# Kernel optimization log

Hardware: AMD Instinct MI355X
Metric: run time of the kernel (lower is better)

Reference implementation:

```python
import jax, jax.numpy as jnp
import numpy as np

N = 100000      # rows of edge_features / scatter dim_size
E = 1000000     # edges
C_IN = 16
C_OUT = 16
H = 32
DIM = 3
RADIUS = 1.0
EPS = 1e-5


def setup_inputs() -> dict:
    key = jax.random.key(0)
    ks = jax.random.split(key, 8)
    s1 = 1.0 / np.sqrt(DIM)
    s2 = 1.0 / np.sqrt(H)
    return {
        "in_edges": jax.random.randint(ks[0], (E,), 0, N, dtype=jnp.int32),
        "out_edges": jax.random.randint(ks[1], (E,), 0, N, dtype=jnp.int32),
        "edge_features": jax.random.normal(ks[2], (N, C_IN), dtype=jnp.float32),
        "hood_coords": jax.random.normal(ks[3], (E, DIM), dtype=jnp.float32),
        "W1": jax.random.normal(ks[4], (DIM, H), dtype=jnp.float32) * s1,
        "b1": jnp.zeros((H,), jnp.float32),
        "g1": jnp.ones((H,), jnp.float32),
        "beta1": jnp.zeros((H,), jnp.float32),
        "W2": jax.random.normal(ks[5], (H, H), dtype=jnp.float32) * s2,
        "b2": jnp.zeros((H,), jnp.float32),
        "g2": jnp.ones((H,), jnp.float32),
        "beta2": jnp.zeros((H,), jnp.float32),
        "W3": jax.random.normal(ks[6], (H, C_IN * C_OUT), dtype=jnp.float32) * s2,
        "b3": jnp.zeros((C_IN * C_OUT,), jnp.float32),
    }


def _layernorm(x, g, b):
    m = jnp.mean(x, axis=-1, keepdims=True)
    v = jnp.mean((x - m) ** 2, axis=-1, keepdims=True)
    return (x - m) * jax.lax.rsqrt(v + EPS) * g + b


def reference(in_edges, out_edges, edge_features, hood_coords,
              W1, b1, g1, beta1, W2, b2, g2, beta2, W3, b3):
    # neural field: coords -> per-edge weight matrix [E, C_OUT, C_IN]
    x = hood_coords / RADIUS
    x = jax.nn.relu(_layernorm(x @ W1 + b1, g1, beta1))
    x = jax.nn.relu(_layernorm(x @ W2 + b2, g2, beta2))
    w = jnp.tanh(x @ W3 + b3).reshape(-1, C_OUT, C_IN)
    # gather + per-edge matvec
    f = edge_features[in_edges]                      # [E, C_IN]
    out_ch = jnp.einsum('ni,noi->no', f, w)          # [E, C_OUT]
    # scatter_mean over out_edges with dim_size = N
    sums = jax.ops.segment_sum(out_ch, out_edges, num_segments=N)
    counts = jax.ops.segment_sum(jnp.ones((out_ch.shape[0],), out_ch.dtype),
                                 out_edges, num_segments=N)
    return sums / jnp.maximum(counts, 1.0)[:, None]
```

## Files before the change

kernel.cpp:

```cpp
#include <hip/hip_runtime.h>
#include <hip/hip_bf16.h>


typedef __attribute__((ext_vector_type(4))) short short4v;
typedef __attribute__((ext_vector_type(4))) float float4v;
typedef __attribute__((ext_vector_type(4))) unsigned uint4v;
typedef __attribute__((ext_vector_type(2))) unsigned uint2v;

constexpr float LN_EPS   = 1e-5f;
constexpr float LOG2E_X2 = 2.8853900817779268f;

__device__ __forceinline__ unsigned f2bf(float x) {
  unsigned u = __builtin_bit_cast(unsigned, x);
  u += 0x7FFFu + ((u >> 16) & 1u);
  return u >> 16;
}
__device__ __forceinline__ unsigned pack2(float lo, float hi) {
  return f2bf(lo) | (f2bf(hi) << 16);
}
__device__ __forceinline__ unsigned packc(float lo, float hi) {
  float2 v; v.x = lo; v.y = hi;
  const __hip_bfloat162 b = __float22bfloat162_rn(v);
  static_assert(sizeof(__hip_bfloat162) == 4, "bf16x2 must be 4 bytes");
  unsigned r;
  __builtin_memcpy(&r, &b, 4);
  return r;
}
__device__ __forceinline__ float bflo2f(unsigned u) {
  return __builtin_bit_cast(float, u << 16);
}
__device__ __forceinline__ float bfhi2f(unsigned u) {
  return __builtin_bit_cast(float, u & 0xFFFF0000u);
}

__device__ __forceinline__ float4v mfma16(short4v a, short4v b, float4v c) {
#if __has_builtin(__builtin_amdgcn_mfma_f32_16x16x16bf16_1k)
  return __builtin_amdgcn_mfma_f32_16x16x16bf16_1k(a, b, c, 0, 0, 0);
#else
  float4v d;
  asm volatile("v_mfma_f32_16x16x16_bf16 %0, %1, %2, %3\n\ts_nop 7\n\ts_nop 7"
               : "=&v"(d) : "v"(a), "v"(b), "v"(c));
  return d;
#endif
}

__device__ __forceinline__ void ln_relu_pack(const float* hv, uint4v gp,
                                             uint4v bp, short4v* bh) {
  float sum = 0.f, ss = 0.f;
#pragma unroll
  for (int s = 0; s < 8; ++s) { sum += hv[s]; ss += hv[s] * hv[s]; }
  sum += __shfl_xor(sum, 16);  ss += __shfl_xor(ss, 16);
  sum += __shfl_xor(sum, 32);  ss += __shfl_xor(ss, 32);
  const float m   = sum * (1.0f / 32.0f);
  const float var = fmaxf(ss * (1.0f / 32.0f) - m * m, 0.f);
  const float rs  = rsqrtf(var + LN_EPS);
#pragma unroll
  for (int h = 0; h < 2; ++h) {
    float y[4];
#pragma unroll
    for (int j = 0; j < 4; ++j) {
      const int s = h * 4 + j;
      const float g  = (s & 1) ? bfhi2f(gp[s >> 1]) : bflo2f(gp[s >> 1]);
      const float be = (s & 1) ? bfhi2f(bp[s >> 1]) : bflo2f(bp[s >> 1]);
      y[j] = fmaxf((hv[s] - m) * rs * g + be, 0.f);
    }
    uint2v u;
    u[0] = packc(y[0], y[1]);
    u[1] = packc(y[2], y[3]);
    bh[h] = __builtin_bit_cast(short4v, u);
  }
}


__global__ void nf_hist(const int* __restrict__ out_edges, int* __restrict__ counts, int E) {
  const int t4 = (blockIdx.x * blockDim.x + threadIdx.x) * 4;
  if (t4 + 3 < E) {
    const int4 v = *(const int4*)(out_edges + t4);
    atomicAdd(&counts[v.x], 1);
    atomicAdd(&counts[v.y], 1);
    atomicAdd(&counts[v.z], 1);
    atomicAdd(&counts[v.w], 1);
  } else {
    for (int i = t4; i < E; ++i) atomicAdd(&counts[out_edges[i]], 1);
  }
}

__global__ void nf_alloc(const int* __restrict__ counts, int* __restrict__ offsets,
                         int* __restrict__ cursor, int* __restrict__ total, int N) {
  const int i = blockIdx.x * blockDim.x + threadIdx.x;
  const int lane = threadIdx.x & 63;
  int c = (i < N) ? counts[i] : 0;
  int sc = c;
#pragma unroll
  for (int d = 1; d < 64; d <<= 1) {
    int v = __shfl_up(sc, d);
    if (lane >= d) sc += v;
  }
  const int excl = sc - c;
  const int wtot = __shfl(sc, 63);
  int base = 0;
  if (lane == 0) base = atomicAdd(total, wtot);
  base = __shfl(base, 0);
  if (i < N) {
    offsets[i] = base + excl;
    cursor[i]  = base + excl;
  }
}


template <int SCATTER_MODE>
__global__ __launch_bounds__(256, 2)
void nf_main(const int* __restrict__ in_edges,
             const int* __restrict__ out_edges,
             const float* __restrict__ ef,
             const float* __restrict__ coords,
             const float* __restrict__ W1, const float* __restrict__ b1,
             const float* __restrict__ g1, const float* __restrict__ be1,
             const float* __restrict__ W2, const float* __restrict__ b2,
             const float* __restrict__ g2, const float* __restrict__ be2,
             const float* __restrict__ W3, const float* __restrict__ b3,
             void* __restrict__ out_ch,
             int* __restrict__ aux,
             int* __restrict__ cursor,
             int E, int ntiles)
{
  __shared__ __align__(16) unsigned sA3[16 * 64 * 4];
  __shared__ __align__(16) float    sB3f[16 * 4 * 4];
  __shared__ __align__(16) unsigned sC1[4][16];
  __shared__ __align__(16) unsigned sC2[4][16];
  __shared__ __align__(16) unsigned sC3[4][4];

  const int t    = threadIdx.x;
  const int l    = t & 63;
  const int q    = l >> 4;
  const int ecol = l & 15;

#pragma unroll
  for (int rep = 0; rep < 4; ++rep) {
    const int idx = rep * 256 + t;
    const int o = idx >> 6, ll = idx & 63;
    const int qq = ll >> 4, ec = ll & 15;
    uint4v w;
#pragma unroll
    for (int h = 0; h < 2; ++h)
#pragma unroll
      for (int jp = 0; jp < 2; ++jp) {
        const float lo = LOG2E_X2 * W3[(4 * qq + 2 * jp     + 16 * h) * 256 + o * 16 + ec];
        const float hi = LOG2E_X2 * W3[(4 * qq + 2 * jp + 1 + 16 * h) * 256 + o * 16 + ec];
        w[h * 2 + jp] = pack2(lo, hi);
      }
    *(uint4v*)&sA3[idx * 4] = w;
  }
  if (t < 64) {
    const int o = t >> 2, qq = t & 3;
    float4v bb;
#pragma unroll
    for (int r = 0; r < 4; ++r) bb[r] = LOG2E_X2 * b3[o * 16 + 4 * qq + r];
    *(float4v*)&sB3f[t * 4] = bb;
  }
  if (t < 4) {
    const int qq = t;
#pragma unroll
    for (int i = 0; i < 4; ++i) {
      const int base = (i < 2) ? (4 * qq + 2 * i) : (4 * qq + 16 + 2 * (i - 2));
      sC1[qq][i]      = pack2(W1[base],      W1[base + 1]);
      sC1[qq][4 + i]  = pack2(W1[32 + base], W1[33 + base]);
      sC1[qq][8 + i]  = pack2(W1[64 + base], W1[65 + base]);
      sC1[qq][12 + i] = pack2(b1[base],      b1[base + 1]);
      sC2[qq][i]      = pack2(g1[base],      g1[base + 1]);
      sC2[qq][4 + i]  = pack2(be1[base],     be1[base + 1]);
      sC2[qq][8 + i]  = pack2(g2[base],      g2[base + 1]);
      sC2[qq][12 + i] = pack2(be2[base],     be2[base + 1]);
      sC3[qq][i]      = pack2(b2[base],      b2[base + 1]);
    }
  }

  short4v a2[2][2];
#pragma unroll
  for (int t2 = 0; t2 < 2; ++t2)
#pragma unroll
    for (int h = 0; h < 2; ++h) {
      short4v v;
#pragma unroll
      for (int j = 0; j < 4; ++j)
        v[j] = (short)f2bf(W2[(4 * q + j + 16 * h) * 32 + ecol + 16 * t2]);
      a2[t2][h] = v;
    }

  __syncthreads();

  auto front = [&](float x0, float x1, float x2, short4v* bh) {
    const uint4v w1r0 = *(const uint4v*)&sC1[q][0];
    const uint4v w1r1 = *(const uint4v*)&sC1[q][4];
    const uint4v w1r2 = *(const uint4v*)&sC1[q][8];
    const uint4v b1v  = *(const uint4v*)&sC1[q][12];
    float hv[8];
#pragma unroll
    for (int i = 0; i < 4; ++i) {
      hv[2 * i]     = bflo2f(b1v[i]) + x0 * bflo2f(w1r0[i])
                    + x1 * bflo2f(w1r1[i]) + x2 * bflo2f(w1r2[i]);
      hv[2 * i + 1] = bfhi2f(b1v[i]) + x0 * bfhi2f(w1r0[i])
                    + x1 * bfhi2f(w1r1[i]) + x2 * bfhi2f(w1r2[i]);
    }
    {
      const uint4v g1v  = *(const uint4v*)&sC2[q][0];
      const uint4v be1v = *(const uint4v*)&sC2[q][4];
      ln_relu_pack(hv, g1v, be1v, bh);
    }
    {
      const uint4v b2v = *(const uint4v*)&sC3[q][0];
#pragma unroll
      for (int t2 = 0; t2 < 2; ++t2) {
        float4v c;
        c[0] = bflo2f(b2v[t2 * 2]);     c[1] = bfhi2f(b2v[t2 * 2]);
        c[2] = bflo2f(b2v[t2 * 2 + 1]); c[3] = bfhi2f(b2v[t2 * 2 + 1]);
        c = mfma16(a2[t2][0], bh[0], c);
        c = mfma16(a2[t2][1], bh[1], c);
        hv[t2 * 4 + 0] = c[0]; hv[t2 * 4 + 1] = c[1];
        hv[t2 * 4 + 2] = c[2]; hv[t2 * 4 + 3] = c[3];
      }
    }
    {
      const uint4v g2v  = *(const uint4v*)&sC2[q][8];
      const uint4v be2v = *(const uint4v*)&sC2[q][12];
      ln_relu_pack(hv, g2v, be2v, bh);
    }
  };

  const int gwave  = (blockIdx.x * blockDim.x + t) >> 6;
  const int nwaves = (gridDim.x * blockDim.x) >> 6;

  int tile = gwave;
  bool validC = false; int oeC = 0;
  short4v bhC[2] = {};
  float4v f4C = {};
  bool validN = false; int ieN = 0, oeN = 0;
  float xN0 = 0.f, xN1 = 0.f, xN2 = 0.f;

  if (tile < ntiles) {
    const int eI = tile * 16 + ecol;
    validC = eI < E;
    const int eS = validC ? eI : 0;
    const int ie = in_edges[eS]; oeC = out_edges[eS];
    const float x0 = coords[3 * eS], x1 = coords[3 * eS + 1], x2 = coords[3 * eS + 2];
    f4C = *(const float4v*)(ef + (size_t)ie * 16 + 4 * q);
    front(x0, x1, x2, bhC);
  }
  if (tile + nwaves < ntiles) {
    const int eI = (tile + nwaves) * 16 + ecol;
    validN = eI < E;
    const int eS = validN ? eI : 0;
    ieN = in_edges[eS]; oeN = out_edges[eS];
    xN0 = coords[3 * eS]; xN1 = coords[3 * eS + 1]; xN2 = coords[3 * eS + 2];
  }

  for (; tile < ntiles; tile += nwaves) {
    const int tn  = tile + nwaves;
    const int tnn = tile + 2 * nwaves;

    float4v f4N = {};
    if (tn < ntiles)
      f4N = *(const float4v*)(ef + (size_t)ieN * 16 + 4 * q);

    int pos = 0;
    if (SCATTER_MODE == 0 && q == 0 && validC)
      pos = atomicAdd(&cursor[oeC], 1);

    bool validNN = false; int ieNN = 0, oeNN = 0;
    float xNN0 = 0.f, xNN1 = 0.f, xNN2 = 0.f;
    if (tnn < ntiles) {
      const int eI = tnn * 16 + ecol;
      validNN = eI < E;
      const int eS = validNN ? eI : 0;
      ieNN = in_edges[eS]; oeNN = out_edges[eS];
      xNN0 = coords[3 * eS]; xNN1 = coords[3 * eS + 1]; xNN2 = coords[3 * eS + 2];
    }

    short4v bhN[2] = {};
    if (tn < ntiles)
      front(xN0, xN1, xN2, bhN);

    const float sumf = (f4C[0] + f4C[1]) + (f4C[2] + f4C[3]);
#pragma unroll
    for (int og = 0; og < 4; ++og) {
      float pr[4];
#pragma unroll
      for (int r = 0; r < 4; ++r) {
        const int o = og * 4 + r;
        const uint4v av = *(const uint4v*)&sA3[(o * 64 + l) * 4];
        float4v c = *(const float4v*)&sB3f[(o * 4 + q) * 4];
        uint2v t0; t0[0] = av[0]; t0[1] = av[1];
        uint2v t1; t1[0] = av[2]; t1[1] = av[3];
        const short4v a30 = __builtin_bit_cast(short4v, t0);
        const short4v a31 = __builtin_bit_cast(short4v, t1);
        c = mfma16(a30, bhC[0], c);
        c = mfma16(a31, bhC[1], c);
        float dot = 0.f;
#pragma unroll
        for (int j = 0; j < 4; ++j) {
          const float e = __builtin_amdgcn_exp2f(c[j]);
          dot = fmaf(f4C[j], __builtin_amdgcn_rcpf(e + 1.0f), dot);
        }
        pr[r] = fmaf(-2.0f, dot, sumf);
      }
#pragma unroll
      for (int r = 0; r < 4; ++r) {
        pr[r] += __shfl_xor(pr[r], 16);
        pr[r] += __shfl_xor(pr[r], 32);
      }
      if (SCATTER_MODE == 0) {
        if (q == 0 && validC) {
          uint2v s;
          s[0] = packc(pr[0], pr[1]);
          s[1] = packc(pr[2], pr[3]);
          *(uint2v*)((unsigned*)out_ch + (size_t)pos * 8 + og * 2) = s;
        }
      } else {
        if (q == 0 && validC) {
          float* sums = (float*)out_ch;
#pragma unroll
          for (int r = 0; r < 4; ++r)
            atomicAdd(&sums[(size_t)oeC * 16 + og * 4 + r], pr[r]);
        }
      }
    }
    if (SCATTER_MODE == 1) {
      if (q == 0 && validC) atomicAdd(&aux[oeC], 1);
    }

    bhC[0] = bhN[0]; bhC[1] = bhN[1];
    f4C = f4N; oeC = oeN; validC = validN;
    ieN = ieNN; oeN = oeNN; validN = validNN;
    xN0 = xNN0; xN1 = xNN1; xN2 = xNN2;
  }
}


__global__ __launch_bounds__(256)
void nf_reduce(const uint4v* __restrict__ out_chb4, const int* __restrict__ counts,
               const int* __restrict__ offsets, float* __restrict__ out, int N) {
  const int gid  = blockIdx.x * 128 + (threadIdx.x >> 1);
  const int half = threadIdx.x & 1;
  if (gid >= N) return;
  const int deg = counts[gid];
  const int off = offsets[gid];
  float a[8] = {0.f, 0.f, 0.f, 0.f, 0.f, 0.f, 0.f, 0.f};
  for (int d = 0; d < deg; ++d) {
    const uint4v u = out_chb4[(size_t)(off + d) * 2 + half];
#pragma unroll
    for (int p = 0; p < 4; ++p) {
      a[2 * p]     += bflo2f(u[p]);
      a[2 * p + 1] += bfhi2f(u[p]);
    }
  }
  const float inv = 1.0f / fmaxf((float)deg, 1.0f);
  float4v r0, r1;
#pragma unroll
  for (int p = 0; p < 4; ++p) { r0[p] = a[p] * inv; r1[p] = a[4 + p] * inv; }
  float* dst = out + (size_t)gid * 16 + 8 * half;
  *(float4v*)dst       = r0;
  *(float4v*)(dst + 4) = r1;
}

__global__ void nf_final(float* __restrict__ out, const int* __restrict__ counts, int n) {
  int i = blockIdx.x * blockDim.x + threadIdx.x;
  if (i < n) {
    float c = (float)counts[i >> 4];
    out[i] = out[i] / fmaxf(c, 1.0f);
  }
}

extern "C" void kernel_launch(void* const* d_in, const int* in_sizes, int n_in,
                              void* d_out, int out_size, void* d_ws, size_t ws_size,
                              hipStream_t stream) {
  const int*   in_edges  = (const int*)d_in[0];
  const int*   out_edges = (const int*)d_in[1];
  const float* ef        = (const float*)d_in[2];
  const float* coords    = (const float*)d_in[3];
  const float* W1  = (const float*)d_in[4];
  const float* b1  = (const float*)d_in[5];
  const float* g1  = (const float*)d_in[6];
  const float* be1 = (const float*)d_in[7];
  const float* W2  = (const float*)d_in[8];
  const float* b2  = (const float*)d_in[9];
  const float* g2  = (const float*)d_in[10];
  const float* be2 = (const float*)d_in[11];
  const float* W3  = (const float*)d_in[12];
  const float* b3  = (const float*)d_in[13];

  const int E = in_sizes[0];
  const int N = in_sizes[2] / 16;
  const int ntiles = (E + 15) / 16;
  float* out = (float*)d_out;

  const size_t need = ((size_t)E * 8 + 3 * (size_t)N + 1) * 4;

  if (ws_size >= need) {
    unsigned* out_chb = (unsigned*)d_ws;
    int*      counts  = (int*)(out_chb + (size_t)E * 8);
    int*      total   = counts + N;
    int*      offsets = total + 1;
    int*      cursor  = offsets + N;

    (void)hipMemsetAsync(counts, 0, ((size_t)N + 1) * sizeof(int), stream);
    nf_hist<<<(E / 4 + 255) / 256 + 1, 256, 0, stream>>>(out_edges, counts, E);
    nf_alloc<<<(N + 255) / 256, 256, 0, stream>>>(counts, offsets, cursor, total, N);
    nf_main<0><<<1024, 256, 0, stream>>>(in_edges, out_edges, ef, coords,
                                         W1, b1, g1, be1, W2, b2, g2, be2, W3, b3,
                                         out_chb, nullptr, cursor, E, ntiles);
    nf_reduce<<<(N + 127) / 128, 256, 0, stream>>>((const uint4v*)out_chb, counts,
                                                   offsets, out, N);
  } else {
    int* counts = (int*)d_ws;
    (void)hipMemsetAsync(out, 0, (size_t)out_size * sizeof(float), stream);
    (void)hipMemsetAsync(counts, 0, (size_t)N * sizeof(int), stream);
    nf_main<1><<<1024, 256, 0, stream>>>(in_edges, out_edges, ef, coords,
                                         W1, b1, g1, be1, W2, b2, g2, be2, W3, b3,
                                         out, counts, nullptr, E, ntiles);
    nf_final<<<(out_size + 255) / 256, 256, 0, stream>>>(out, counts, out_size);
  }
}
```

Measured before the change: 211.1 us.

## Switch neural-field MLP to 32x32x8 MFMA with 32-edge tiles

Recasts the per-edge MLP and the W3 weight generation from 16x16x16 bf16 MFMA on 16-edge tiles to 32x32x8 MFMA on 32-edge tiles. Shared-memory layouts for W3, biases and the LayerNorm constants are rearranged to match, and the cross-lane reductions drop from two shuffles to one. The software pipeline becomes shallower: the two-stage prefetch of indices, coords and features and the precomputed next-tile front end are replaced by a single-stage prefetch. The larger accumulators raise register pressure, and the shallower pipeline exposes more load latency.

```diff
diff --git a/kernel.cpp b/kernel.cpp
--- a/kernel.cpp
+++ b/kernel.cpp
@@ -2,10 +2,11 @@
 #include <hip/hip_bf16.h>
 
 
-typedef __attribute__((ext_vector_type(4))) short short4v;
-typedef __attribute__((ext_vector_type(4))) float float4v;
-typedef __attribute__((ext_vector_type(4))) unsigned uint4v;
-typedef __attribute__((ext_vector_type(2))) unsigned uint2v;
+typedef __attribute__((ext_vector_type(4)))  short    short4v;
+typedef __attribute__((ext_vector_type(4)))  float    float4v;
+typedef __attribute__((ext_vector_type(16))) float    f32x16;
+typedef __attribute__((ext_vector_type(4)))  unsigned uint4v;
+typedef __attribute__((ext_vector_type(2)))  unsigned uint2v;
 
 constexpr float LN_EPS   = 1e-5f;
 constexpr float LOG2E_X2 = 2.8853900817779268f;
@@ -32,42 +33,41 @@
 __device__ __forceinline__ float bfhi2f(unsigned u) {
   return __builtin_bit_cast(float, u & 0xFFFF0000u);
 }
-
-__device__ __forceinline__ float4v mfma16(short4v a, short4v b, float4v c) {
-#if __has_builtin(__builtin_amdgcn_mfma_f32_16x16x16bf16_1k)
-  return __builtin_amdgcn_mfma_f32_16x16x16bf16_1k(a, b, c, 0, 0, 0);
+__device__ __forceinline__ float sigm2(float x) {
+  return __builtin_amdgcn_rcpf(__builtin_amdgcn_exp2f(x) + 1.0f);
+}
+
+__device__ __forceinline__ f32x16 mfma32(short4v a, short4v b, f32x16 c) {
+#if __has_builtin(__builtin_amdgcn_mfma_f32_32x32x8bf16_1k)
+  return __builtin_amdgcn_mfma_f32_32x32x8bf16_1k(a, b, c, 0, 0, 0);
 #else
-  float4v d;
-  asm volatile("v_mfma_f32_16x16x16_bf16 %0, %1, %2, %3\n\ts_nop 7\n\ts_nop 7"
-               : "=&v"(d) : "v"(a), "v"(b), "v"(c));
-  return d;
+  asm volatile("v_mfma_f32_32x32x8_bf16 %0, %1, %2, %0\n\ts_nop 7\n\ts_nop 7"
+               : "+v"(c) : "v"(a), "v"(b));
+  return c;
 #endif
 }
 
-__device__ __forceinline__ void ln_relu_pack(const float* hv, uint4v gp,
-                                             uint4v bp, short4v* bh) {
+__device__ __forceinline__ void ln_relu_pack32(const float* hv, const unsigned* gp,
+                                               const unsigned* bp, short4v* bh) {
   float sum = 0.f, ss = 0.f;
 #pragma unroll
-  for (int s = 0; s < 8; ++s) { sum += hv[s]; ss += hv[s] * hv[s]; }
-  sum += __shfl_xor(sum, 16);  ss += __shfl_xor(ss, 16);
-  sum += __shfl_xor(sum, 32);  ss += __shfl_xor(ss, 32);
+  for (int i = 0; i < 16; ++i) { sum += hv[i]; ss += hv[i] * hv[i]; }
+  sum += __shfl_xor(sum, 32);
+  ss  += __shfl_xor(ss, 32);
   const float m   = sum * (1.0f / 32.0f);
   const float var = fmaxf(ss * (1.0f / 32.0f) - m * m, 0.f);
   const float rs  = rsqrtf(var + LN_EPS);
 #pragma unroll
-  for (int h = 0; h < 2; ++h) {
+  for (int s = 0; s < 4; ++s) {
     float y[4];
 #pragma unroll
-    for (int j = 0; j < 4; ++j) {
-      const int s = h * 4 + j;
-      const float g  = (s & 1) ? bfhi2f(gp[s >> 1]) : bflo2f(gp[s >> 1]);
-      const float be = (s & 1) ? bfhi2f(bp[s >> 1]) : bflo2f(bp[s >> 1]);
-      y[j] = fmaxf((hv[s] - m) * rs * g + be, 0.f);
-    }
-    uint2v u;
-    u[0] = packc(y[0], y[1]);
-    u[1] = packc(y[2], y[3]);
-    bh[h] = __builtin_bit_cast(short4v, u);
+    for (int p = 0; p < 2; ++p) {
+      const unsigned g = gp[s * 2 + p], b = bp[s * 2 + p];
+      y[2 * p]     = fmaxf((hv[s * 4 + 2 * p]     - m) * rs * bflo2f(g) + bflo2f(b), 0.f);
+      y[2 * p + 1] = fmaxf((hv[s * 4 + 2 * p + 1] - m) * rs * bfhi2f(g) + bfhi2f(b), 0.f);
+    }
+    uint2v u; u[0] = packc(y[0], y[1]); u[1] = packc(y[2], y[3]);
+    bh[s] = __builtin_bit_cast(short4v, u);
   }
 }
 
@@ -124,214 +124,216 @@
              int* __restrict__ cursor,
              int E, int ntiles)
 {
-  __shared__ __align__(16) unsigned sA3[16 * 64 * 4];
-  __shared__ __align__(16) float    sB3f[16 * 4 * 4];
-  __shared__ __align__(16) unsigned sC1[4][16];
-  __shared__ __align__(16) unsigned sC2[4][16];
-  __shared__ __align__(16) unsigned sC3[4][4];
+  __shared__ __align__(16) unsigned sA3[8 * 2 * 64 * 4];
+  __shared__ __align__(16) float    sB3f[256];
+  __shared__ __align__(16) unsigned sK[2][64];
+  __shared__ __align__(16) float    sB2f[2][16];
 
   const int t    = threadIdx.x;
   const int l    = t & 63;
-  const int q    = l >> 4;
-  const int ecol = l & 15;
-
-#pragma unroll
-  for (int rep = 0; rep < 4; ++rep) {
+  const int h    = l >> 5;
+  const int ecol = l & 31;
+
+#pragma unroll
+  for (int rep = 0; rep < 16; ++rep) {
     const int idx = rep * 256 + t;
-    const int o = idx >> 6, ll = idx & 63;
-    const int qq = ll >> 4, ec = ll & 15;
-    uint4v w;
-#pragma unroll
-    for (int h = 0; h < 2; ++h)
-#pragma unroll
-      for (int jp = 0; jp < 2; ++jp) {
-        const float lo = LOG2E_X2 * W3[(4 * qq + 2 * jp     + 16 * h) * 256 + o * 16 + ec];
-        const float hi = LOG2E_X2 * W3[(4 * qq + 2 * jp + 1 + 16 * h) * 256 + o * 16 + ec];
-        w[h * 2 + jp] = pack2(lo, hi);
-      }
-    *(uint4v*)&sA3[idx * 4] = w;
-  }
-  if (t < 64) {
-    const int o = t >> 2, qq = t & 3;
-    float4v bb;
-#pragma unroll
-    for (int r = 0; r < 4; ++r) bb[r] = LOG2E_X2 * b3[o * 16 + 4 * qq + r];
-    *(float4v*)&sB3f[t * 4] = bb;
-  }
-  if (t < 4) {
-    const int qq = t;
-#pragma unroll
-    for (int i = 0; i < 4; ++i) {
-      const int base = (i < 2) ? (4 * qq + 2 * i) : (4 * qq + 16 + 2 * (i - 2));
-      sC1[qq][i]      = pack2(W1[base],      W1[base + 1]);
-      sC1[qq][4 + i]  = pack2(W1[32 + base], W1[33 + base]);
-      sC1[qq][8 + i]  = pack2(W1[64 + base], W1[65 + base]);
-      sC1[qq][12 + i] = pack2(b1[base],      b1[base + 1]);
-      sC2[qq][i]      = pack2(g1[base],      g1[base + 1]);
-      sC2[qq][4 + i]  = pack2(be1[base],     be1[base + 1]);
-      sC2[qq][8 + i]  = pack2(g2[base],      g2[base + 1]);
-      sC2[qq][12 + i] = pack2(be2[base],     be2[base + 1]);
-      sC3[qq][i]      = pack2(b2[base],      b2[base + 1]);
-    }
-  }
-
-  short4v a2[2][2];
-#pragma unroll
-  for (int t2 = 0; t2 < 2; ++t2)
-#pragma unroll
-    for (int h = 0; h < 2; ++h) {
-      short4v v;
-#pragma unroll
-      for (int j = 0; j < 4; ++j)
-        v[j] = (short)f2bf(W2[(4 * q + j + 16 * h) * 32 + ecol + 16 * t2]);
-      a2[t2][h] = v;
-    }
-
+    const int u = idx & 3, ll = (idx >> 2) & 63, b = (idx >> 8) & 1, mt = idx >> 9;
+    const int s = b * 2 + (u >> 1), jp = u & 1;
+    const int hh = ll >> 5, m = ll & 31;
+    const int o = 2 * mt + (m >> 4), i = m & 15;
+    const int k0 = 8 * s + 4 * hh + 2 * jp;
+    sA3[idx] = pack2(LOG2E_X2 * W3[(size_t)k0 * 256 + o * 16 + i],
+                     LOG2E_X2 * W3[(size_t)(k0 + 1) * 256 + o * 16 + i]);
+  }
+  sB3f[t] = LOG2E_X2 * b3[t];
+  if (t < 128) {
+    const int hh = t >> 6, i = t & 63;
+    const int sp = i & 7;
+    const int ch = 8 * (sp >> 1) + 4 * hh + 2 * (sp & 1);
+    if (i < 24) {
+      const int d = i >> 3;
+      sK[hh][i] = pack2(W1[d * 32 + ch], W1[d * 32 + ch + 1]);
+    } else {
+      const float* src = (i < 32) ? b1 : (i < 40) ? g1 : (i < 48) ? be1
+                        : (i < 56) ? g2 : be2;
+      sK[hh][i] = pack2(src[ch], src[ch + 1]);
+    }
+  }
+  if (t < 32) {
+    const int hh = t >> 4, r = t & 15;
+    sB2f[hh][r] = b2[(r & 3) + 8 * (r >> 2) + 4 * hh];
+  }
+
+  short4v a2[4];
+#pragma unroll
+  for (int s = 0; s < 4; ++s) {
+    short4v v;
+#pragma unroll
+    for (int j = 0; j < 4; ++j)
+      v[j] = (short)f2bf(W2[(8 * s + 4 * h + j) * 32 + ecol]);
+    a2[s] = v;
+  }
   __syncthreads();
-
-  auto front = [&](float x0, float x1, float x2, short4v* bh) {
-    const uint4v w1r0 = *(const uint4v*)&sC1[q][0];
-    const uint4v w1r1 = *(const uint4v*)&sC1[q][4];
-    const uint4v w1r2 = *(const uint4v*)&sC1[q][8];
-    const uint4v b1v  = *(const uint4v*)&sC1[q][12];
-    float hv[8];
-#pragma unroll
-    for (int i = 0; i < 4; ++i) {
-      hv[2 * i]     = bflo2f(b1v[i]) + x0 * bflo2f(w1r0[i])
-                    + x1 * bflo2f(w1r1[i]) + x2 * bflo2f(w1r2[i]);
-      hv[2 * i + 1] = bfhi2f(b1v[i]) + x0 * bfhi2f(w1r0[i])
-                    + x1 * bfhi2f(w1r1[i]) + x2 * bfhi2f(w1r2[i]);
-    }
-    {
-      const uint4v g1v  = *(const uint4v*)&sC2[q][0];
-      const uint4v be1v = *(const uint4v*)&sC2[q][4];
-      ln_relu_pack(hv, g1v, be1v, bh);
-    }
-    {
-      const uint4v b2v = *(const uint4v*)&sC3[q][0];
-#pragma unroll
-      for (int t2 = 0; t2 < 2; ++t2) {
-        float4v c;
-        c[0] = bflo2f(b2v[t2 * 2]);     c[1] = bfhi2f(b2v[t2 * 2]);
-        c[2] = bflo2f(b2v[t2 * 2 + 1]); c[3] = bfhi2f(b2v[t2 * 2 + 1]);
-        c = mfma16(a2[t2][0], bh[0], c);
-        c = mfma16(a2[t2][1], bh[1], c);
-        hv[t2 * 4 + 0] = c[0]; hv[t2 * 4 + 1] = c[1];
-        hv[t2 * 4 + 2] = c[2]; hv[t2 * 4 + 3] = c[3];
-      }
-    }
-    {
-      const uint4v g2v  = *(const uint4v*)&sC2[q][8];
-      const uint4v be2v = *(const uint4v*)&sC2[q][12];
-      ln_relu_pack(hv, g2v, be2v, bh);
-    }
-  };
 
   const int gwave  = (blockIdx.x * blockDim.x + t) >> 6;
   const int nwaves = (gridDim.x * blockDim.x) >> 6;
 
   int tile = gwave;
-  bool validC = false; int oeC = 0;
-  short4v bhC[2] = {};
-  float4v f4C = {};
-  bool validN = false; int ieN = 0, oeN = 0;
-  float xN0 = 0.f, xN1 = 0.f, xN2 = 0.f;
-
+  bool valid = false; int oe = 0;
+  float x0 = 0.f, x1 = 0.f, x2 = 0.f;
+  float4v f4a = {}, f4b = {};
   if (tile < ntiles) {
-    const int eI = tile * 16 + ecol;
-    validC = eI < E;
-    const int eS = validC ? eI : 0;
-    const int ie = in_edges[eS]; oeC = out_edges[eS];
-    const float x0 = coords[3 * eS], x1 = coords[3 * eS + 1], x2 = coords[3 * eS + 2];
-    f4C = *(const float4v*)(ef + (size_t)ie * 16 + 4 * q);
-    front(x0, x1, x2, bhC);
-  }
-  if (tile + nwaves < ntiles) {
-    const int eI = (tile + nwaves) * 16 + ecol;
-    validN = eI < E;
-    const int eS = validN ? eI : 0;
-    ieN = in_edges[eS]; oeN = out_edges[eS];
-    xN0 = coords[3 * eS]; xN1 = coords[3 * eS + 1]; xN2 = coords[3 * eS + 2];
+    const int eIdx = tile * 32 + ecol;
+    valid = eIdx < E;
+    const int eS = valid ? eIdx : 0;
+    const int ie = in_edges[eS]; oe = out_edges[eS];
+    x0 = coords[3 * eS]; x1 = coords[3 * eS + 1]; x2 = coords[3 * eS + 2];
+    f4a = *(const float4v*)(ef + (size_t)ie * 16 + 4 * h);
+    f4b = *(const float4v*)(ef + (size_t)ie * 16 + 8 + 4 * h);
   }
 
   for (; tile < ntiles; tile += nwaves) {
-    const int tn  = tile + nwaves;
-    const int tnn = tile + 2 * nwaves;
-
-    float4v f4N = {};
-    if (tn < ntiles)
-      f4N = *(const float4v*)(ef + (size_t)ieN * 16 + 4 * q);
+    const int tn = tile + nwaves;
+    int ieN = 0, oeN = 0; bool validN = false;
+    float x0N = 0.f, x1N = 0.f, x2N = 0.f;
+    if (tn < ntiles) {
+      const int eIdxN = tn * 32 + ecol;
+      validN = eIdxN < E;
+      const int eSN = validN ? eIdxN : 0;
+      ieN = in_edges[eSN]; oeN = out_edges[eSN];
+      x0N = coords[3 * eSN]; x1N = coords[3 * eSN + 1]; x2N = coords[3 * eSN + 2];
+    }
 
     int pos = 0;
-    if (SCATTER_MODE == 0 && q == 0 && validC)
-      pos = atomicAdd(&cursor[oeC], 1);
-
-    bool validNN = false; int ieNN = 0, oeNN = 0;
-    float xNN0 = 0.f, xNN1 = 0.f, xNN2 = 0.f;
-    if (tnn < ntiles) {
-      const int eI = tnn * 16 + ecol;
-      validNN = eI < E;
-      const int eS = validNN ? eI : 0;
-      ieNN = in_edges[eS]; oeNN = out_edges[eS];
-      xNN0 = coords[3 * eS]; xNN1 = coords[3 * eS + 1]; xNN2 = coords[3 * eS + 2];
-    }
-
-    short4v bhN[2] = {};
-    if (tn < ntiles)
-      front(xN0, xN1, xN2, bhN);
-
-    const float sumf = (f4C[0] + f4C[1]) + (f4C[2] + f4C[3]);
-#pragma unroll
-    for (int og = 0; og < 4; ++og) {
-      float pr[4];
-#pragma unroll
-      for (int r = 0; r < 4; ++r) {
-        const int o = og * 4 + r;
-        const uint4v av = *(const uint4v*)&sA3[(o * 64 + l) * 4];
-        float4v c = *(const float4v*)&sB3f[(o * 4 + q) * 4];
-        uint2v t0; t0[0] = av[0]; t0[1] = av[1];
-        uint2v t1; t1[0] = av[2]; t1[1] = av[3];
-        const short4v a30 = __builtin_bit_cast(short4v, t0);
-        const short4v a31 = __builtin_bit_cast(short4v, t1);
-        c = mfma16(a30, bhC[0], c);
-        c = mfma16(a31, bhC[1], c);
-        float dot = 0.f;
-#pragma unroll
-        for (int j = 0; j < 4; ++j) {
-          const float e = __builtin_amdgcn_exp2f(c[j]);
-          dot = fmaf(f4C[j], __builtin_amdgcn_rcpf(e + 1.0f), dot);
+    if (SCATTER_MODE == 0 && h == 0 && valid)
+      pos = atomicAdd(&cursor[oe], 1);
+
+    float hv[16];
+    {
+      const uint4v* kk = (const uint4v*)&sK[h][0];
+      const uint4v b1a = kk[6], b1b = kk[7];
+#pragma unroll
+      for (int sp = 0; sp < 8; ++sp) {
+        const unsigned ub = (sp < 4) ? b1a[sp] : b1b[sp - 4];
+        const int base = (sp >> 1) * 4 + (sp & 1) * 2;
+        hv[base]     = bflo2f(ub);
+        hv[base + 1] = bfhi2f(ub);
+      }
+#pragma unroll
+      for (int d = 0; d < 3; ++d) {
+        const uint4v wa = kk[d * 2], wb = kk[d * 2 + 1];
+        const float xd = (d == 0) ? x0 : (d == 1) ? x1 : x2;
+#pragma unroll
+        for (int sp = 0; sp < 8; ++sp) {
+          const unsigned uw = (sp < 4) ? wa[sp] : wb[sp - 4];
+          const int base = (sp >> 1) * 4 + (sp & 1) * 2;
+          hv[base]     = fmaf(xd, bflo2f(uw), hv[base]);
+          hv[base + 1] = fmaf(xd, bfhi2f(uw), hv[base + 1]);
         }
-        pr[r] = fmaf(-2.0f, dot, sumf);
-      }
-#pragma unroll
-      for (int r = 0; r < 4; ++r) {
-        pr[r] += __shfl_xor(pr[r], 16);
-        pr[r] += __shfl_xor(pr[r], 32);
-      }
+      }
+    }
+    short4v bh[4];
+    {
+      unsigned lnc[16];
+      const uint4v* kg = (const uint4v*)&sK[h][32];
+#pragma unroll
+      for (int r4 = 0; r4 < 4; ++r4) {
+        const uint4v v = kg[r4];
+        lnc[r4 * 4 + 0] = v[0]; lnc[r4 * 4 + 1] = v[1];
+        lnc[r4 * 4 + 2] = v[2]; lnc[r4 * 4 + 3] = v[3];
+      }
+      ln_relu_pack32(hv, &lnc[0], &lnc[8], bh);
+    }
+
+    f32x16 c;
+    {
+      const float4v* bb = (const float4v*)&sB2f[h][0];
+      const float4v c0 = bb[0], c1 = bb[1], c2 = bb[2], c3i = bb[3];
+#pragma unroll
+      for (int e = 0; e < 4; ++e) {
+        c[e] = c0[e]; c[4 + e] = c1[e]; c[8 + e] = c2[e]; c[12 + e] = c3i[e];
+      }
+    }
+#pragma unroll
+    for (int s = 0; s < 4; ++s) c = mfma32(a2[s], bh[s], c);
+
+    {
+      float hv2[16];
+#pragma unroll
+      for (int r = 0; r < 16; ++r) hv2[r] = c[r];
+      unsigned ln2[16];
+      const uint4v* kg2 = (const uint4v*)&sK[h][48];
+#pragma unroll
+      for (int r4 = 0; r4 < 4; ++r4) {
+        const uint4v v = kg2[r4];
+        ln2[r4 * 4 + 0] = v[0]; ln2[r4 * 4 + 1] = v[1];
+        ln2[r4 * 4 + 2] = v[2]; ln2[r4 * 4 + 3] = v[3];
+      }
+      ln_relu_pack32(hv2, &ln2[0], &ln2[8], bh);
+    }
+
+    float4v f4aN = {}, f4bN = {};
+    if (tn < ntiles) {
+      f4aN = *(const float4v*)(ef + (size_t)ieN * 16 + 4 * h);
+      f4bN = *(const float4v*)(ef + (size_t)ieN * 16 + 8 + 4 * h);
+    }
+
+    const float sumf = (f4a[0] + f4a[1]) + (f4a[2] + f4a[3])
+                     + (f4b[0] + f4b[1]) + (f4b[2] + f4b[3]);
+
+#pragma unroll
+    for (int mt = 0; mt < 8; ++mt) {
+      const uint4v av0 = *(const uint4v*)&sA3[mt * 512 + (l << 2)];
+      const uint4v av1 = *(const uint4v*)&sA3[mt * 512 + 256 + (l << 2)];
+      f32x16 c3;
+      {
+        const float4v i0 = *(const float4v*)&sB3f[(2 * mt) * 16 + 4 * h];
+        const float4v i1 = *(const float4v*)&sB3f[(2 * mt) * 16 + 8 + 4 * h];
+        const float4v i2 = *(const float4v*)&sB3f[(2 * mt + 1) * 16 + 4 * h];
+        const float4v i3 = *(const float4v*)&sB3f[(2 * mt + 1) * 16 + 8 + 4 * h];
+#pragma unroll
+        for (int e = 0; e < 4; ++e) {
+          c3[e] = i0[e]; c3[4 + e] = i1[e]; c3[8 + e] = i2[e]; c3[12 + e] = i3[e];
+        }
+      }
+      uint2v u01, u23;
+      u01[0] = av0[0]; u01[1] = av0[1];  u23[0] = av0[2]; u23[1] = av0[3];
+      c3 = mfma32(__builtin_bit_cast(short4v, u01), bh[0], c3);
+      c3 = mfma32(__builtin_bit_cast(short4v, u23), bh[1], c3);
+      u01[0] = av1[0]; u01[1] = av1[1];  u23[0] = av1[2]; u23[1] = av1[3];
+      c3 = mfma32(__builtin_bit_cast(short4v, u01), bh[2], c3);
+      c3 = mfma32(__builtin_bit_cast(short4v, u23), bh[3], c3);
+
+      float dot0 = 0.f, dot1 = 0.f;
+#pragma unroll
+      for (int j = 0; j < 4; ++j) {
+        dot0 = fmaf(f4a[j], sigm2(c3[j]),      dot0);
+        dot0 = fmaf(f4b[j], sigm2(c3[4 + j]),  dot0);
+        dot1 = fmaf(f4a[j], sigm2(c3[8 + j]),  dot1);
+        dot1 = fmaf(f4b[j], sigm2(c3[12 + j]), dot1);
+      }
+      float pr0 = fmaf(-2.0f, dot0, sumf);
+      float pr1 = fmaf(-2.0f, dot1, sumf);
+      pr0 += __shfl_xor(pr0, 32);
+      pr1 += __shfl_xor(pr1, 32);
+
       if (SCATTER_MODE == 0) {
-        if (q == 0 && validC) {
-          uint2v s;
-          s[0] = packc(pr[0], pr[1]);
-          s[1] = packc(pr[2], pr[3]);
-          *(uint2v*)((unsigned*)out_ch + (size_t)pos * 8 + og * 2) = s;
+        if (h == 0 && valid)
+          ((unsigned*)out_ch)[(size_t)pos * 8 + mt] = packc(pr0, pr1);
+      } else {
+        if (h == 0 && valid) {
+          float* sums = (float*)out_ch;
+          atomicAdd(&sums[(size_t)oe * 16 + 2 * mt],     pr0);
+          atomicAdd(&sums[(size_t)oe * 16 + 2 * mt + 1], pr1);
         }
-      } else {
-        if (q == 0 && validC) {
-          float* sums = (float*)out_ch;
-#pragma unroll
-          for (int r = 0; r < 4; ++r)
-            atomicAdd(&sums[(size_t)oeC * 16 + og * 4 + r], pr[r]);
-        }
       }
     }
     if (SCATTER_MODE == 1) {
-      if (q == 0 && validC) atomicAdd(&aux[oeC], 1);
-    }
-
-    bhC[0] = bhN[0]; bhC[1] = bhN[1];
-    f4C = f4N; oeC = oeN; validC = validN;
-    ieN = ieNN; oeN = oeNN; validN = validNN;
-    xN0 = xNN0; xN1 = xNN1; xN2 = xNN2;
+      if (h == 0 && valid) atomicAdd(&aux[oe], 1);
+    }
+
+    valid = validN; oe = oeN;
+    x0 = x0N; x1 = x1N; x2 = x2N; f4a = f4aN; f4b = f4bN;
   }
 }
 
@@ -390,7 +392,7 @@
 
   const int E = in_sizes[0];
   const int N = in_sizes[2] / 16;
-  const int ntiles = (E + 15) / 16;
+  const int ntiles = (E + 31) / 32;
   float* out = (float*)d_out;
 
   const size_t need = ((size_t)E * 8 + 3 * (size_t)N + 1) * 4;
```

Result: slower. 533.4 us (+152.7%).
